# Optimization experiments

Hardware: AMD Instinct MI355X
Metric: run time of the kernel (lower is better)

## Reference

```python
import jax, jax.numpy as jnp
import numpy as np

N_NODES = 50000
N_EDGES = 800000
N_GRAPHS = 64
D = 64            # input_dim == hidden_dim == output_dim
N_GIN = 4         # num_layers - 1 GINConv layers
N_PRED = 5        # num_layers prediction heads
BN_EPS = 1e-5


def setup_inputs() -> dict:
    key = jax.random.key(0)
    ks = jax.random.split(key, 12)
    x = jax.random.normal(ks[0], (N_NODES, D), dtype=jnp.float32)
    edge_index = jax.random.randint(ks[1], (2, N_EDGES), 0, N_NODES, dtype=jnp.int32)
    # contiguous graph ids covering all N_GRAPHS segments (PyG batch vector)
    batch = ((jnp.arange(N_NODES) * N_GRAPHS) // N_NODES).astype(jnp.int32)
    s = 1.0 / np.sqrt(D)
    mlp_W1 = jax.random.uniform(ks[2], (N_GIN, D, D), jnp.float32, -s, s)
    mlp_b1 = jax.random.uniform(ks[3], (N_GIN, D), jnp.float32, -s, s)
    mlp_W2 = jax.random.uniform(ks[4], (N_GIN, D, D), jnp.float32, -s, s)
    mlp_b2 = jax.random.uniform(ks[5], (N_GIN, D), jnp.float32, -s, s)
    bn_gamma = jnp.ones((N_GIN, D), jnp.float32)
    bn_beta = jnp.zeros((N_GIN, D), jnp.float32)
    prelu_alpha = jnp.float32(0.25)  # nn.PReLU default, shared across layers
    pred_W = jax.random.uniform(ks[6], (N_PRED, D, D), jnp.float32, -s, s)
    pred_b = jax.random.uniform(ks[7], (N_PRED, D), jnp.float32, -s, s)
    return {
        "x": x, "edge_index": edge_index, "batch": batch,
        "mlp_W1": mlp_W1, "mlp_b1": mlp_b1, "mlp_W2": mlp_W2, "mlp_b2": mlp_b2,
        "bn_gamma": bn_gamma, "bn_beta": bn_beta, "prelu_alpha": prelu_alpha,
        "pred_W": pred_W, "pred_b": pred_b,
    }


def reference(x, edge_index, batch, mlp_W1, mlp_b1, mlp_W2, mlp_b2,
              bn_gamma, bn_beta, prelu_alpha, pred_W, pred_b):
    src, dst = edge_index[0], edge_index[1]
    h = x
    hidden_rep = [h]
    for l in range(N_GIN):
        # GINConv, eps = 0 (learn_eps=False): (1+eps)*x_i + sum_{j->i} x_j
        agg = jax.ops.segment_sum(h[src], dst, num_segments=N_NODES)
        z = h + agg
        # 2-layer MLP: Linear -> ReLU -> Linear
        z = jax.nn.relu(z @ mlp_W1[l] + mlp_b1[l])
        z = z @ mlp_W2[l] + mlp_b2[l]
        # BatchNorm1d over nodes (training-mode batch stats)
        mean = z.mean(axis=0)
        var = z.var(axis=0)
        z = (z - mean) * jax.lax.rsqrt(var + BN_EPS) * bn_gamma[l] + bn_beta[l]
        # shared single-parameter PReLU
        h = jnp.where(z > 0, z, prelu_alpha * z)
        hidden_rep.append(h)
    # per-layer max graph pooling + linear head (dropout_prob=0 -> identity)
    reps = []
    for l, hr in enumerate(hidden_rep):
        pooled = jax.ops.segment_max(hr, batch, num_segments=N_GRAPHS)
        reps.append(pooled @ pred_W[l] + pred_b[l])
    # torch.stack(dim=-1) -> (B, D, L), 'cat' aggregation flattens to (B, D*L)
    return jnp.stack(reps, axis=-1).reshape(N_GRAPHS, -1)
```

## Files before the change

### kernel.cpp

```cpp
#include <hip/hip_runtime.h>
#include <hip/hip_bf16.h>

#define N_NODES 50000
#define N_EDGES 800000
#define N_GRAPHS 64
#define DIM 64
#define N_GIN 4
#define N_PRED 5
#define BN_EPS 1e-5f
#define MM_BLOCKS 782
#define NB 625
#define BUCKET_SZ 80
#define POOL_CH 16

typedef short bf16x8 __attribute__((ext_vector_type(8)));
typedef float f32x4 __attribute__((ext_vector_type(4)));

__device__ __forceinline__ float b2f(__hip_bfloat16 v) { return __bfloat162float(v); }

__device__ __forceinline__ float loadv(const void* p, size_t i, int isb) {
    return isb ? b2f(((const __hip_bfloat16*)p)[i]) : ((const float*)p)[i];
}

__device__ __forceinline__ unsigned short f2bu(float f) {
    __hip_bfloat16 h = __float2bfloat16(f);
    return *(unsigned short*)&h;
}
__device__ __forceinline__ float bu2f(unsigned short u) {
    __hip_bfloat16 h = *(__hip_bfloat16*)&u;
    return b2f(h);
}

__device__ __forceinline__ unsigned int enc_f(float f) {
    unsigned int b = __float_as_uint(f);
    return (b & 0x80000000u) ? ~b : (b | 0x80000000u);
}
__device__ __forceinline__ float dec_f(unsigned int u) {
    unsigned int b = (u & 0x80000000u) ? (u ^ 0x80000000u) : ~u;
    return __uint_as_float(b);
}

__device__ __forceinline__ unsigned int gstart(unsigned int g) {
    return (g * (unsigned int)N_NODES + (N_GRAPHS - 1)) >> 6;
}
__device__ __forceinline__ unsigned int graph_of(unsigned int row) {
    return (row * (unsigned int)N_GRAPHS) / (unsigned int)N_NODES;
}

__global__ void init_all(unsigned int* __restrict__ base, int nZero, int nTotal,
                         const unsigned int* __restrict__ xw, int* __restrict__ flag) {
    int idx = blockIdx.x * blockDim.x + threadIdx.x;
    if (idx < nZero) base[idx] = 0u;
    else if (idx < nTotal) base[idx] = 0xFFFFFFFFu;
    if (blockIdx.x == 0) {
        __shared__ int cnt[256];
        int t = threadIdx.x;
        int c = 0;
        for (int i = t; i < 1024; i += 256) {
            unsigned int e = (xw[i] >> 7) & 0xFFu;
            if (e >= 0x70u && e <= 0x85u) c++;
        }
        cnt[t] = c;
        __syncthreads();
        for (int s = 128; s > 0; s >>= 1) {
            if (t < s) cnt[t] += cnt[t + s];
            __syncthreads();
        }
        if (t == 0) *flag = (cnt[0] >= 512) ? 1 : 0;
    }
}

__global__ void zero_u32(unsigned int* __restrict__ p, int n) {
    int i = blockIdx.x * blockDim.x + threadIdx.x;
    if (i < n) p[i] = 0u;
}

__global__ __launch_bounds__(256) void convert_pool_bg(
    const void* __restrict__ x, unsigned short* __restrict__ H,
    unsigned int* __restrict__ poolEnc, const int* __restrict__ dflag) {
    __shared__ float shmx[4][64];
    int isb = *dflag;
    unsigned int g = blockIdx.x / POOL_CH, p = blockIdx.x % POOL_CH;
    unsigned int s = gstart(g), e = gstart(g + 1), len = e - s;
    unsigned int rs = s + (len * p) / POOL_CH, re = s + (len * (p + 1)) / POOL_CH;
    int r = threadIdx.x >> 6, c = threadIdx.x & 63;
    float mx = -3.0e38f;
    for (unsigned int row = rs + r; row < re; row += 4) {
        float v = loadv(x, (size_t)row * DIM + c, isb);
        H[(size_t)row * DIM + c] = f2bu(v);
        mx = fmaxf(mx, v);
    }
    shmx[r][c] = mx;
    __syncthreads();
    if (threadIdx.x < 64) {
        float m = fmaxf(fmaxf(shmx[0][c], shmx[1][c]), fmaxf(shmx[2][c], shmx[3][c]));
        atomicMax(&poolEnc[g * DIM + c], enc_f(m));
    }
}


__global__ __launch_bounds__(256) void bucket_hist(const int* __restrict__ dst,
                                                   unsigned int* __restrict__ bucketCnt) {
    __shared__ unsigned int h[NB];
    for (int i = threadIdx.x; i < NB; i += 256) h[i] = 0u;
    __syncthreads();
    for (int e = blockIdx.x * 256 + threadIdx.x; e < N_EDGES; e += gridDim.x * 256)
        atomicAdd(&h[(unsigned int)dst[e] / BUCKET_SZ], 1u);
    __syncthreads();
    for (int i = threadIdx.x; i < NB; i += 256) {
        unsigned int v = h[i];
        if (v) atomicAdd(&bucketCnt[i], v);
    }
}

__global__ void scan_buckets(const unsigned int* __restrict__ bucketCnt,
                             unsigned int* __restrict__ bucketBase,
                             unsigned int* __restrict__ bucketCur) {
    __shared__ unsigned int s[256];
    int t = threadIdx.x;
    int i0 = t * 3;
    unsigned int v0 = (i0 < NB) ? bucketCnt[i0] : 0u;
    unsigned int v1 = (i0 + 1 < NB) ? bucketCnt[i0 + 1] : 0u;
    unsigned int v2 = (i0 + 2 < NB) ? bucketCnt[i0 + 2] : 0u;
    unsigned int tsum = v0 + v1 + v2;
    s[t] = tsum;
    __syncthreads();
    for (int off = 1; off < 256; off <<= 1) {
        unsigned int u = (t >= off) ? s[t - off] : 0u;
        __syncthreads();
        s[t] += u;
        __syncthreads();
    }
    unsigned int ex = s[t] - tsum;
    if (i0 < NB)     { bucketBase[i0] = ex;          bucketCur[i0] = ex; }
    if (i0 + 1 < NB) { bucketBase[i0 + 1] = ex + v0; bucketCur[i0 + 1] = ex + v0; }
    if (i0 + 2 < NB) { bucketBase[i0 + 2] = ex + v0 + v1; bucketCur[i0 + 2] = ex + v0 + v1; }
}

__global__ __launch_bounds__(256) void bucket_scatter(
    const int* __restrict__ src, const int* __restrict__ dst,
    unsigned int* __restrict__ bucketCur, uint2* __restrict__ ebuf) {
    __shared__ unsigned int h[NB];
    __shared__ unsigned int base[NB];
    for (int i = threadIdx.x; i < NB; i += 256) h[i] = 0u;
    __syncthreads();
    for (int e = blockIdx.x * 256 + threadIdx.x; e < N_EDGES; e += gridDim.x * 256)
        atomicAdd(&h[(unsigned int)dst[e] / BUCKET_SZ], 1u);
    __syncthreads();
    for (int i = threadIdx.x; i < NB; i += 256) {
        unsigned int v = h[i];
        base[i] = v ? atomicAdd(&bucketCur[i], v) : 0u;
        h[i] = 0u;
    }
    __syncthreads();
    for (int e = blockIdx.x * 256 + threadIdx.x; e < N_EDGES; e += gridDim.x * 256) {
        unsigned int d = (unsigned int)dst[e];
        unsigned int b = d / BUCKET_SZ;
        unsigned int off = atomicAdd(&h[b], 1u);
        ebuf[base[b] + off] = make_uint2((unsigned int)src[e], d);
    }
}

__global__ __launch_bounds__(256) void bucket_csr(
    const uint2* __restrict__ ebuf, const unsigned int* __restrict__ bucketBase,
    const unsigned int* __restrict__ bucketCnt, unsigned int* __restrict__ deg,
    unsigned int* __restrict__ cur, unsigned int* __restrict__ srclist) {
    __shared__ unsigned int ldeg[BUCKET_SZ], lcur[BUCKET_SZ], lscan[BUCKET_SZ];
    int b = blockIdx.x;
    unsigned int ebase = bucketBase[b];
    unsigned int ecnt = bucketCnt[b];
    unsigned int nbase = (unsigned int)b * BUCKET_SZ;
    int t = threadIdx.x;
    if (t < BUCKET_SZ) ldeg[t] = 0u;
    __syncthreads();
    for (unsigned int i = t; i < ecnt; i += 256)
        atomicAdd(&ldeg[ebuf[ebase + i].y - nbase], 1u);
    __syncthreads();
    if (t < BUCKET_SZ) lscan[t] = ldeg[t];
    __syncthreads();
    for (int off = 1; off < BUCKET_SZ; off <<= 1) {
        unsigned int u = 0u;
        if (t < BUCKET_SZ && t >= off) u = lscan[t - off];
        __syncthreads();
        if (t < BUCKET_SZ) lscan[t] += u;
        __syncthreads();
    }
    if (t < BUCKET_SZ) {
        lcur[t] = lscan[t] - ldeg[t];
        deg[nbase + t] = ldeg[t];
        cur[nbase + t] = ebase + lscan[t];
    }
    __syncthreads();
    for (unsigned int i = t; i < ecnt; i += 256) {
        uint2 e = ebuf[ebase + i];
        unsigned int off = atomicAdd(&lcur[e.y - nbase], 1u);
        srclist[ebase + off] = e.x;
    }
}


__global__ void pack_w(const void* __restrict__ W1, const void* __restrict__ W2,
                       unsigned short* __restrict__ P, const int* __restrict__ dflag) {
    int isb = *dflag;
    int mi = blockIdx.x;
    const void* src = (mi < 4) ? W1 : W2;
    size_t off = (size_t)(mi & 3) * 4096;
    for (int it = 0; it < 16; it++) {
        int idx = it * 256 + threadIdx.x;
        int j = idx & 7, l = (idx >> 3) & 63, s = (idx >> 9) & 1, t = idx >> 10;
        int k = s * 32 + (l >> 4) * 8 + j;
        int n = t * 16 + (l & 15);
        P[(size_t)mi * 4096 + idx] = f2bu(loadv(src, off + (size_t)k * 64 + n, isb));
    }
}

__global__ __launch_bounds__(256) void gather_affine(
    const unsigned short* __restrict__ Zsrc, unsigned short* __restrict__ Xb,
    const unsigned int* __restrict__ cur, const unsigned int* __restrict__ deg,
    const unsigned int* __restrict__ srclist, const float* __restrict__ scsh,
    const void* __restrict__ alpha_p, int ident, const int* __restrict__ dflag) {
    int lane = threadIdx.x & 63;
    int w = threadIdx.x >> 6;
    int node = blockIdx.x * 4 + w;
    int g8 = lane >> 3;
    int t8 = lane & 7;
    float sc[8], sh[8], alpha;
    if (ident) {
#pragma unroll
        for (int k = 0; k < 8; k++) { sc[k] = 1.0f; sh[k] = 0.0f; }
        alpha = 1.0f;
    } else {
#pragma unroll
        for (int k = 0; k < 8; k++) {
            sc[k] = scsh[t8 * 8 + k];
            sh[k] = scsh[64 + t8 * 8 + k];
        }
        alpha = loadv(alpha_p, 0, *dflag);
    }
    unsigned int cnt = deg[node];
    unsigned int start = cur[node] - cnt;
    const unsigned int* sl = srclist + start;
    float a[8] = {0.f, 0.f, 0.f, 0.f, 0.f, 0.f, 0.f, 0.f};
    if (g8 == 0) {
        bf16x8 sv = *(const bf16x8*)&Zsrc[(size_t)node * DIM + t8 * 8];
#pragma unroll
        for (int k = 0; k < 8; k++) {
            float v = bu2f((unsigned short)sv[k]) * sc[k] + sh[k];
            a[k] = v > 0.0f ? v : alpha * v;
        }
    }
    for (unsigned int j = g8; j < cnt; j += 8) {
        unsigned int s = sl[j];
        bf16x8 v = *(const bf16x8*)&Zsrc[(size_t)s * DIM + t8 * 8];
#pragma unroll
        for (int k = 0; k < 8; k++) {
            float h = bu2f((unsigned short)v[k]) * sc[k] + sh[k];
            a[k] += h > 0.0f ? h : alpha * h;
        }
    }
#pragma unroll
    for (int k = 0; k < 8; k++) {
        a[k] += __shfl_xor(a[k], 8);
        a[k] += __shfl_xor(a[k], 16);
        a[k] += __shfl_xor(a[k], 32);
    }
    if (g8 == 0) {
        bf16x8 o;
#pragma unroll
        for (int k = 0; k < 8; k++) o[k] = (short)f2bu(a[k]);
        *(bf16x8*)&Xb[(size_t)node * DIM + t8 * 8] = o;
    }
}

template <bool WRITEZ>
__global__ __launch_bounds__(256) void fused_mm(
    const unsigned short* __restrict__ Xb,
    const unsigned short* __restrict__ P1, const unsigned short* __restrict__ P2,
    const void* __restrict__ b1, size_t b1Off, const void* __restrict__ b2, size_t b2Off,
    unsigned short* __restrict__ Zb, float* __restrict__ part,
    unsigned int* __restrict__ zmaxE, unsigned int* __restrict__ zminE,
    const int* __restrict__ dflag) {
    __shared__ __align__(16) short T2[4][16][72];
    __shared__ float S1[4][64], S2[4][64];
    __shared__ unsigned int zmxL[2][64], zmnL[2][64];
    int isb = *dflag;
    int tid = threadIdx.x;
    int lane = tid & 63;
    int w = tid >> 6;
    if (tid < 128) {
        zmxL[tid >> 6][tid & 63] = 0u;
        zmnL[tid >> 6][tid & 63] = 0xFFFFFFFFu;
    }
    __syncthreads();
    int r0 = blockIdx.x * 64 + w * 16;
    bool valid = (r0 < N_NODES);
    int m = lane & 15, q = lane >> 4;
    int row = valid ? (r0 + m) : m;
    int r0blk = blockIdx.x * 64;
    unsigned int gLo = graph_of((unsigned int)r0blk);
    int lastRow = r0blk + 63 > N_NODES - 1 ? N_NODES - 1 : r0blk + 63;
    unsigned int gHi = graph_of((unsigned int)lastRow);

    const bf16x8* Xv = (const bf16x8*)Xb;
    bf16x8 a0 = Xv[(size_t)row * 8 + q];
    bf16x8 a1 = Xv[(size_t)row * 8 + 4 + q];
    const bf16x8* P1v = (const bf16x8*)P1;
    const bf16x8* P2v = (const bf16x8*)P2;
    bf16x8 w1[8], w2[8];
#pragma unroll
    for (int i = 0; i < 8; i++) {
        w1[i] = P1v[(size_t)i * 64 + lane];
        w2[i] = P2v[(size_t)i * 64 + lane];
    }

    f32x4 acc[4] = {{0.f, 0.f, 0.f, 0.f}, {0.f, 0.f, 0.f, 0.f},
                    {0.f, 0.f, 0.f, 0.f}, {0.f, 0.f, 0.f, 0.f}};
#pragma unroll
    for (int t = 0; t < 4; t++) {
        acc[t] = __builtin_amdgcn_mfma_f32_16x16x32_bf16(a0, w1[t * 2 + 0], acc[t], 0, 0, 0);
        acc[t] = __builtin_amdgcn_mfma_f32_16x16x32_bf16(a1, w1[t * 2 + 1], acc[t], 0, 0, 0);
    }
#pragma unroll
    for (int t = 0; t < 4; t++) {
        int col = t * 16 + m;
        float bv = loadv(b1, b1Off + col, isb);
#pragma unroll
        for (int reg = 0; reg < 4; reg++) {
            float v = acc[t][reg] + bv;
            v = v > 0.0f ? v : 0.0f;
            T2[w][q * 4 + reg][col] = (short)f2bu(v);
        }
    }

    bf16x8 c0 = *(const bf16x8*)&T2[w][m][q * 8];
    bf16x8 c1 = *(const bf16x8*)&T2[w][m][32 + q * 8];
    f32x4 acc2[4] = {{0.f, 0.f, 0.f, 0.f}, {0.f, 0.f, 0.f, 0.f},
                     {0.f, 0.f, 0.f, 0.f}, {0.f, 0.f, 0.f, 0.f}};
#pragma unroll
    for (int t = 0; t < 4; t++) {
        acc2[t] = __builtin_amdgcn_mfma_f32_16x16x32_bf16(c0, w2[t * 2 + 0], acc2[t], 0, 0, 0);
        acc2[t] = __builtin_amdgcn_mfma_f32_16x16x32_bf16(c1, w2[t * 2 + 1], acc2[t], 0, 0, 0);
    }

    float s1[4], s2[4];
#pragma unroll
    for (int t = 0; t < 4; t++) {
        float a = 0.0f, b = 0.0f;
        if (valid) {
            int col = t * 16 + m;
            float bv = loadv(b2, b2Off + col, isb);
            int rbase = r0 + q * 4;
#pragma unroll
            for (int reg = 0; reg < 4; reg++) {
                float z = acc2[t][reg] + bv;
                if (WRITEZ) Zb[(size_t)(rbase + reg) * DIM + col] = f2bu(z);
                unsigned int e = enc_f(z);
                unsigned int gi = graph_of((unsigned int)(rbase + reg)) - gLo;
                atomicMax(&zmxL[gi][col], e);
                atomicMin(&zmnL[gi][col], e);
                a += z;
                b += z * z;
            }
        }
        s1[t] = a;
        s2[t] = b;
    }
#pragma unroll
    for (int t = 0; t < 4; t++) {
        s1[t] += __shfl_xor(s1[t], 16);
        s1[t] += __shfl_xor(s1[t], 32);
        s2[t] += __shfl_xor(s2[t], 16);
        s2[t] += __shfl_xor(s2[t], 32);
    }
    if (q == 0) {
#pragma unroll
        for (int t = 0; t < 4; t++) {
            S1[w][t * 16 + m] = s1[t];
            S2[w][t * 16 + m] = s2[t];
        }
    }
    __syncthreads();
    if (tid < 128) {
        int c = tid & 63;
        float v = (tid < 64) ? (S1[0][c] + S1[1][c] + S1[2][c] + S1[3][c])
                             : (S2[0][c] + S2[1][c] + S2[2][c] + S2[3][c]);
        part[(size_t)blockIdx.x * 128 + tid] = v;
        int gi = tid >> 6;
        if (gLo + gi <= gHi) {
            atomicMax(&zmaxE[(gLo + gi) * 64 + c], zmxL[gi][c]);
            atomicMin(&zminE[(gLo + gi) * 64 + c], zmnL[gi][c]);
        }
    }
}

__global__ void stats_finalize(const float* __restrict__ part,
                               const void* __restrict__ gamma, const void* __restrict__ beta,
                               size_t gOff, float* __restrict__ scsh,
                               const int* __restrict__ dflag) {
    __shared__ double sh1[256], sh2[256];
    int c = blockIdx.x;
    int t = threadIdx.x;
    double a1 = 0.0, a2 = 0.0;
    for (int b = t; b < MM_BLOCKS; b += 256) {
        a1 += (double)part[(size_t)b * 128 + c];
        a2 += (double)part[(size_t)b * 128 + 64 + c];
    }
    sh1[t] = a1;
    sh2[t] = a2;
    __syncthreads();
    for (int s = 128; s > 0; s >>= 1) {
        if (t < s) { sh1[t] += sh1[t + s]; sh2[t] += sh2[t + s]; }
        __syncthreads();
    }
    if (t == 0) {
        int isb = *dflag;
        double mean = sh1[0] * (1.0 / N_NODES);
        double var = sh2[0] * (1.0 / N_NODES) - mean * mean;
        float inv = rsqrtf(fmaxf((float)var, 0.0f) + BN_EPS);
        float g = loadv(gamma, gOff + c, isb);
        float bb = loadv(beta, gOff + c, isb);
        scsh[c] = g * inv;
        scsh[64 + c] = bb - (float)mean * g * inv;
    }
}


__global__ void convert_pool_f(const void* __restrict__ x, float* __restrict__ A,
                               const int* __restrict__ batch,
                               unsigned int* __restrict__ poolEnc,
                               const int* __restrict__ dflag) {
    int isb = *dflag;
    int idx = blockIdx.x * blockDim.x + threadIdx.x;
    if (idx >= N_NODES * DIM) return;
    int i = idx >> 6, c = idx & 63;
    float v = loadv(x, idx, isb);
    A[idx] = v;
    atomicMax(&poolEnc[batch[i] * DIM + c], enc_f(v));
}

__global__ void copy_f4(const float4* __restrict__ A, float4* __restrict__ B, int n4) {
    int i = blockIdx.x * blockDim.x + threadIdx.x;
    if (i < n4) B[i] = A[i];
}

__global__ void edge_scatter(const int* __restrict__ src, const int* __restrict__ dst,
                             const float* __restrict__ A, float* __restrict__ B) {
    int idx = blockIdx.x * blockDim.x + threadIdx.x;
    if (idx >= N_EDGES * 16) return;
    int e = idx >> 4, q = idx & 15;
    int s = src[e], d = dst[e];
    float4 v = ((const float4*)(A + (size_t)s * DIM))[q];
    float* bp = B + (size_t)d * DIM + (q << 2);
    atomicAdd(bp + 0, v.x);
    atomicAdd(bp + 1, v.y);
    atomicAdd(bp + 2, v.z);
    atomicAdd(bp + 3, v.w);
}

template <bool RELU, bool STATS>
__global__ void mm64(const float* __restrict__ X, const void* __restrict__ W, size_t wOff,
                     const void* __restrict__ bias, size_t bOff, float* __restrict__ Y,
                     double* __restrict__ stats, const int* __restrict__ dflag) {
    int isb = *dflag;
    __shared__ float Ws[64][64];
    __shared__ float Xs[4][64];
    __shared__ float Sv[4][64];
    __shared__ float bsh[64];
    int tid = threadIdx.x;
    for (int i = tid; i < 4096; i += 256) Ws[i >> 6][i & 63] = loadv(W, wOff + i, isb);
    if (tid < 64) bsh[tid] = loadv(bias, bOff + tid, isb);
    int r = tid >> 6, d = tid & 63;
    int row = blockIdx.x * 4 + r;
    Xs[r][d] = X[(size_t)row * DIM + d];
    __syncthreads();
    float acc = bsh[d];
#pragma unroll
    for (int k = 0; k < 64; k++) acc += Xs[r][k] * Ws[k][d];
    if (RELU) acc = acc > 0.0f ? acc : 0.0f;
    Y[(size_t)row * DIM + d] = acc;
    if (STATS) {
        Sv[r][d] = acc;
        __syncthreads();
        if (tid < 64) {
            float s = 0.0f, s2 = 0.0f;
#pragma unroll
            for (int rr = 0; rr < 4; rr++) {
                float v = Sv[rr][tid];
                s += v;
                s2 += v * v;
            }
            atomicAdd(&stats[tid], (double)s);
            atomicAdd(&stats[64 + tid], (double)s2);
        }
    }
}

__global__ void bn_prelu_pool_f(const float* __restrict__ Z, float* __restrict__ H,
                                const double* __restrict__ stats,
                                const void* __restrict__ gamma, const void* __restrict__ beta,
                                size_t gOff, const void* __restrict__ alpha_p,
                                const int* __restrict__ batch,
                                unsigned int* __restrict__ poolEnc,
                                const int* __restrict__ dflag) {
    int isb = *dflag;
    int idx = blockIdx.x * blockDim.x + threadIdx.x;
    if (idx >= N_NODES * DIM) return;
    int i = idx >> 6, c = idx & 63;
    double mn = stats[c] * (1.0 / N_NODES);
    double var = stats[64 + c] * (1.0 / N_NODES) - mn * mn;
    float inv = rsqrtf(fmaxf((float)var, 0.0f) + BN_EPS);
    float z = Z[idx];
    float v = (z - (float)mn) * inv * loadv(gamma, gOff + c, isb) + loadv(beta, gOff + c, isb);
    float alpha = loadv(alpha_p, 0, isb);
    v = v > 0.0f ? v : alpha * v;
    H[idx] = v;
    atomicMax(&poolEnc[batch[i] * DIM + c], enc_f(v));
}

__global__ void pred_head(const unsigned int* __restrict__ poolEnc,
                          const unsigned int* __restrict__ zmaxE,
                          const unsigned int* __restrict__ zminE,
                          const float* __restrict__ scshAll,
                          const void* __restrict__ alpha_p,
                          const void* __restrict__ predW, const void* __restrict__ predB,
                          void* __restrict__ out, const int* __restrict__ dflag,
                          int useZmm) {
    int isb = *dflag;
    int l = blockIdx.x / N_GRAPHS;
    int g = blockIdx.x % N_GRAPHS;
    int d = threadIdx.x;
    __shared__ float ps[64];
    float pv;
    if (!useZmm || l == 0) {
        pv = dec_f(poolEnc[(size_t)l * N_GRAPHS * DIM + g * DIM + d]);
    } else {
        int s = l - 1;
        float sc = scshAll[s * 128 + d];
        float sh = scshAll[s * 128 + 64 + d];
        float alpha = loadv(alpha_p, 0, isb);
        float t1 = sc * dec_f(zmaxE[(size_t)s * 4096 + g * 64 + d]) + sh;
        float t2 = sc * dec_f(zminE[(size_t)s * 4096 + g * 64 + d]) + sh;
        float h1 = t1 > 0.0f ? t1 : alpha * t1;
        float h2 = t2 > 0.0f ? t2 : alpha * t2;
        pv = fmaxf(h1, h2);
    }
    ps[d] = pv;
    __syncthreads();
    float acc = loadv(predB, (size_t)l * DIM + d, isb);
    size_t wbase = (size_t)l * DIM * DIM;
#pragma unroll
    for (int k = 0; k < 64; k++) acc += ps[k] * loadv(predW, wbase + k * DIM + d, isb);
    int o = g * (DIM * N_PRED) + d * N_PRED + l;
    if (isb) ((__hip_bfloat16*)out)[o] = __float2bfloat16(acc);
    else ((float*)out)[o] = acc;
}

extern "C" void kernel_launch(void* const* d_in, const int* in_sizes, int n_in,
                              void* d_out, int out_size, void* d_ws, size_t ws_size,
                              hipStream_t stream) {
    const void* x     = d_in[0];
    const int*  edge  = (const int*)d_in[1];
    const int*  batch = (const int*)d_in[2];
    const void* W1    = d_in[3];
    const void* b1    = d_in[4];
    const void* W2    = d_in[5];
    const void* b2    = d_in[6];
    const void* gamma = d_in[7];
    const void* beta  = d_in[8];
    const void* alpha = d_in[9];
    const void* pW    = d_in[10];
    const void* pB    = d_in[11];

    float* A = (float*)d_ws;
    float* B = A + (size_t)N_NODES * DIM;
    unsigned int* poolEnc   = (unsigned int*)(B + (size_t)N_NODES * DIM);
    unsigned int* bucketCnt = poolEnc + N_PRED * N_GRAPHS * DIM;
    unsigned int* zmaxE     = bucketCnt + NB;
    unsigned int* zminE     = zmaxE + 4 * 4096;
    int* dflag = (int*)(zminE + 4 * 4096);
    unsigned int* deg        = (unsigned int*)(dflag + 1);
    unsigned int* cur        = deg + N_NODES;
    unsigned int* bucketBase = cur + N_NODES;
    unsigned int* bucketCur  = bucketBase + NB;
    unsigned int* srclist    = bucketCur + NB;
    unsigned short* Wpack = (unsigned short*)(srclist + N_EDGES);
    float* part    = (float*)(Wpack + 8 * 4096);
    float* scshAll = part + (size_t)MM_BLOCKS * 128;
    double* statsF = (double*)(scshAll + 512);
    uint2* ebuf = (uint2*)B;

    size_t needFull = (size_t)((char*)(statsF + 128) - (char*)d_ws);
    bool useMFMA = ws_size >= needFull;

    const int* esrc = edge;
    const int* edst = edge + N_EDGES;
    const int ND = N_NODES * DIM;

    unsigned short* Hb = (unsigned short*)A;
    unsigned short* Xb = Hb + (size_t)N_NODES * DIM;
    unsigned short* Zb = (unsigned short*)B;

    const int initZeroCnt = N_PRED * N_GRAPHS * DIM + NB + 4 * 4096;
    const int initTotCnt  = initZeroCnt + 4 * 4096;
    init_all<<<(initTotCnt + 255) / 256, 256, 0, stream>>>(poolEnc, initZeroCnt, initTotCnt,
                                                           (const unsigned int*)x, dflag);

    if (useMFMA) {
        bucket_hist<<<200, 256, 0, stream>>>(edst, bucketCnt);
        scan_buckets<<<1, 256, 0, stream>>>(bucketCnt, bucketBase, bucketCur);
        bucket_scatter<<<200, 256, 0, stream>>>(esrc, edst, bucketCur, ebuf);
        bucket_csr<<<NB, 256, 0, stream>>>(ebuf, bucketBase, bucketCnt, deg, cur, srclist);

        pack_w<<<8, 256, 0, stream>>>(W1, W2, Wpack, dflag);
        convert_pool_bg<<<N_GRAPHS * POOL_CH, 256, 0, stream>>>(x, Hb, poolEnc, dflag);
        for (int l = 0; l < N_GIN; l++) {
            size_t bOff = (size_t)l * DIM;
            if (l == 0)
                gather_affine<<<N_NODES / 4, 256, 0, stream>>>(
                    Hb, Xb, cur, deg, srclist, nullptr, alpha, 1, dflag);
            else
                gather_affine<<<N_NODES / 4, 256, 0, stream>>>(
                    Zb, Xb, cur, deg, srclist, scshAll + (size_t)(l - 1) * 128, alpha, 0,
                    dflag);
            if (l < 3)
                fused_mm<true><<<MM_BLOCKS, 256, 0, stream>>>(
                    Xb, Wpack + (size_t)l * 4096, Wpack + (size_t)(4 + l) * 4096,
                    b1, bOff, b2, bOff, Zb, part, zmaxE + (size_t)l * 4096,
                    zminE + (size_t)l * 4096, dflag);
            else
                fused_mm<false><<<MM_BLOCKS, 256, 0, stream>>>(
                    Xb, Wpack + (size_t)l * 4096, Wpack + (size_t)(4 + l) * 4096,
                    b1, bOff, b2, bOff, Zb, part, zmaxE + (size_t)l * 4096,
                    zminE + (size_t)l * 4096, dflag);
            stats_finalize<<<64, 256, 0, stream>>>(part, gamma, beta, bOff,
                                                   scshAll + (size_t)l * 128, dflag);
        }
        pred_head<<<N_PRED * N_GRAPHS, DIM, 0, stream>>>(
            poolEnc, zmaxE, zminE, scshAll, alpha, pW, pB, d_out, dflag, 1);
    } else {
        convert_pool_f<<<ND / 256, 256, 0, stream>>>(x, A, batch, poolEnc, dflag);
        for (int l = 0; l < N_GIN; l++) {
            size_t wOff = (size_t)l * DIM * DIM;
            size_t bOff = (size_t)l * DIM;
            copy_f4<<<(ND / 4 + 255) / 256, 256, 0, stream>>>((const float4*)A, (float4*)B,
                                                              ND / 4);
            edge_scatter<<<(N_EDGES * 16) / 256, 256, 0, stream>>>(esrc, edst, A, B);
            mm64<true, false><<<N_NODES / 4, 256, 0, stream>>>(B, W1, wOff, b1, bOff, A, nullptr,
                                                               dflag);
            zero_u32<<<1, 256, 0, stream>>>((unsigned int*)statsF, 256);
            mm64<false, true><<<N_NODES / 4, 256, 0, stream>>>(A, W2, wOff, b2, bOff, B, statsF,
                                                               dflag);
            bn_prelu_pool_f<<<ND / 256, 256, 0, stream>>>(
                B, A, statsF, gamma, beta, bOff, alpha, batch,
                poolEnc + (size_t)(l + 1) * N_GRAPHS * DIM, dflag);
        }
        pred_head<<<N_PRED * N_GRAPHS, DIM, 0, stream>>>(
            poolEnc, zmaxE, zminE, scshAll, alpha, pW, pB, d_out, dflag, 0);
    }
}
```

Before: 310.1 us.

## Split node features into two 32-channel planes and gather each half separately

Node feature buffers (input H and intermediate Z) are stored as two separate 32-channel bf16 planes instead of one interleaved 64-channel array. The gather kernel is launched twice per layer, once per plane, with 16 edge slots per wave and 4 lanes per row. This shrinks the random-access working set per gather pass so more of it can stay in cache. The trade-off is reading the CSR lists twice and issuing smaller, 64-byte row reads.

```diff
diff --git a/kernel.cpp b/kernel.cpp
--- a/kernel.cpp
+++ b/kernel.cpp
@@ -76,8 +76,9 @@
 }
 
 __global__ __launch_bounds__(256) void convert_pool_bg(
-    const void* __restrict__ x, unsigned short* __restrict__ H,
-    unsigned int* __restrict__ poolEnc, const int* __restrict__ dflag) {
+    const void* __restrict__ x, unsigned short* __restrict__ H0,
+    unsigned short* __restrict__ H1, unsigned int* __restrict__ poolEnc,
+    const int* __restrict__ dflag) {
     __shared__ float shmx[4][64];
     int isb = *dflag;
     unsigned int g = blockIdx.x / POOL_CH, p = blockIdx.x % POOL_CH;
@@ -87,7 +88,8 @@
     float mx = -3.0e38f;
     for (unsigned int row = rs + r; row < re; row += 4) {
         float v = loadv(x, (size_t)row * DIM + c, isb);
-        H[(size_t)row * DIM + c] = f2bu(v);
+        if (c < 32) H0[(size_t)row * 32 + c] = f2bu(v);
+        else        H1[(size_t)row * 32 + (c - 32)] = f2bu(v);
         mx = fmaxf(mx, v);
     }
     shmx[r][c] = mx;
@@ -214,16 +216,17 @@
     }
 }
 
-__global__ __launch_bounds__(256) void gather_affine(
-    const unsigned short* __restrict__ Zsrc, unsigned short* __restrict__ Xb,
+__global__ __launch_bounds__(256) void gather_half(
+    const unsigned short* __restrict__ Zp, unsigned short* __restrict__ Xb,
     const unsigned int* __restrict__ cur, const unsigned int* __restrict__ deg,
-    const unsigned int* __restrict__ srclist, const float* __restrict__ scsh,
-    const void* __restrict__ alpha_p, int ident, const int* __restrict__ dflag) {
+    const unsigned int* __restrict__ srclist, const float* __restrict__ scshL,
+    const void* __restrict__ alpha_p, int ident, int chbase,
+    const int* __restrict__ dflag) {
     int lane = threadIdx.x & 63;
     int w = threadIdx.x >> 6;
     int node = blockIdx.x * 4 + w;
-    int g8 = lane >> 3;
-    int t8 = lane & 7;
+    int slot = lane >> 2;
+    int t = lane & 3;
     float sc[8], sh[8], alpha;
     if (ident) {
 #pragma unroll
@@ -232,8 +235,8 @@
     } else {
 #pragma unroll
         for (int k = 0; k < 8; k++) {
-            sc[k] = scsh[t8 * 8 + k];
-            sh[k] = scsh[64 + t8 * 8 + k];
+            sc[k] = scshL[chbase + t * 8 + k];
+            sh[k] = scshL[64 + chbase + t * 8 + k];
         }
         alpha = loadv(alpha_p, 0, *dflag);
     }
@@ -241,17 +244,17 @@
     unsigned int start = cur[node] - cnt;
     const unsigned int* sl = srclist + start;
     float a[8] = {0.f, 0.f, 0.f, 0.f, 0.f, 0.f, 0.f, 0.f};
-    if (g8 == 0) {
-        bf16x8 sv = *(const bf16x8*)&Zsrc[(size_t)node * DIM + t8 * 8];
+    if (slot == 0) {
+        bf16x8 sv = *(const bf16x8*)&Zp[(size_t)node * 32 + t * 8];
 #pragma unroll
         for (int k = 0; k < 8; k++) {
             float v = bu2f((unsigned short)sv[k]) * sc[k] + sh[k];
             a[k] = v > 0.0f ? v : alpha * v;
         }
     }
-    for (unsigned int j = g8; j < cnt; j += 8) {
+    for (unsigned int j = slot; j < cnt; j += 16) {
         unsigned int s = sl[j];
-        bf16x8 v = *(const bf16x8*)&Zsrc[(size_t)s * DIM + t8 * 8];
+        bf16x8 v = *(const bf16x8*)&Zp[(size_t)s * 32 + t * 8];
 #pragma unroll
         for (int k = 0; k < 8; k++) {
             float h = bu2f((unsigned short)v[k]) * sc[k] + sh[k];
@@ -260,15 +263,16 @@
     }
 #pragma unroll
     for (int k = 0; k < 8; k++) {
+        a[k] += __shfl_xor(a[k], 4);
         a[k] += __shfl_xor(a[k], 8);
         a[k] += __shfl_xor(a[k], 16);
         a[k] += __shfl_xor(a[k], 32);
     }
-    if (g8 == 0) {
+    if (slot == 0) {
         bf16x8 o;
 #pragma unroll
         for (int k = 0; k < 8; k++) o[k] = (short)f2bu(a[k]);
-        *(bf16x8*)&Xb[(size_t)node * DIM + t8 * 8] = o;
+        *(bf16x8*)&Xb[(size_t)node * DIM + chbase + t * 8] = o;
     }
 }
 
@@ -350,10 +354,12 @@
             int col = t * 16 + m;
             float bv = loadv(b2, b2Off + col, isb);
             int rbase = r0 + q * 4;
+            unsigned short* Zp = Zb + ((col >= 32) ? (size_t)N_NODES * 32 : 0);
+            int colh = col & 31;
 #pragma unroll
             for (int reg = 0; reg < 4; reg++) {
                 float z = acc2[t][reg] + bv;
-                if (WRITEZ) Zb[(size_t)(rbase + reg) * DIM + col] = f2bu(z);
+                if (WRITEZ) Zp[(size_t)(rbase + reg) * 32 + colh] = f2bu(z);
                 unsigned int e = enc_f(z);
                 unsigned int gi = graph_of((unsigned int)(rbase + reg)) - gLo;
                 atomicMax(&zmxL[gi][col], e);
@@ -596,9 +602,9 @@
     const int* edst = edge + N_EDGES;
     const int ND = N_NODES * DIM;
 
-    unsigned short* Hb = (unsigned short*)A;
-    unsigned short* Xb = Hb + (size_t)N_NODES * DIM;
-    unsigned short* Zb = (unsigned short*)B;
+    unsigned short* Hp = (unsigned short*)A;
+    unsigned short* Xb = Hp + (size_t)N_NODES * DIM;
+    unsigned short* Zp = (unsigned short*)B;
 
     const int initZeroCnt = N_PRED * N_GRAPHS * DIM + NB + 4 * 4096;
     const int initTotCnt  = initZeroCnt + 4 * 4096;
@@ -612,25 +618,27 @@
         bucket_csr<<<NB, 256, 0, stream>>>(ebuf, bucketBase, bucketCnt, deg, cur, srclist);
 
         pack_w<<<8, 256, 0, stream>>>(W1, W2, Wpack, dflag);
-        convert_pool_bg<<<N_GRAPHS * POOL_CH, 256, 0, stream>>>(x, Hb, poolEnc, dflag);
+        convert_pool_bg<<<N_GRAPHS * POOL_CH, 256, 0, stream>>>(
+            x, Hp, Hp + (size_t)N_NODES * 32, poolEnc, dflag);
         for (int l = 0; l < N_GIN; l++) {
             size_t bOff = (size_t)l * DIM;
-            if (l == 0)
-                gather_affine<<<N_NODES / 4, 256, 0, stream>>>(
-                    Hb, Xb, cur, deg, srclist, nullptr, alpha, 1, dflag);
-            else
-                gather_affine<<<N_NODES / 4, 256, 0, stream>>>(
-                    Zb, Xb, cur, deg, srclist, scshAll + (size_t)(l - 1) * 128, alpha, 0,
-                    dflag);
+            const unsigned short* srcPl = (l == 0) ? Hp : Zp;
+            const float* scshL = (l == 0) ? nullptr : scshAll + (size_t)(l - 1) * 128;
+            int ident = (l == 0) ? 1 : 0;
+            gather_half<<<N_NODES / 4, 256, 0, stream>>>(
+                srcPl, Xb, cur, deg, srclist, scshL, alpha, ident, 0, dflag);
+            gather_half<<<N_NODES / 4, 256, 0, stream>>>(
+                srcPl + (size_t)N_NODES * 32, Xb, cur, deg, srclist, scshL, alpha, ident, 32,
+                dflag);
             if (l < 3)
                 fused_mm<true><<<MM_BLOCKS, 256, 0, stream>>>(
                     Xb, Wpack + (size_t)l * 4096, Wpack + (size_t)(4 + l) * 4096,
-                    b1, bOff, b2, bOff, Zb, part, zmaxE + (size_t)l * 4096,
+                    b1, bOff, b2, bOff, Zp, part, zmaxE + (size_t)l * 4096,
                     zminE + (size_t)l * 4096, dflag);
             else
                 fused_mm<false><<<MM_BLOCKS, 256, 0, stream>>>(
                     Xb, Wpack + (size_t)l * 4096, Wpack + (size_t)(4 + l) * 4096,
-                    b1, bOff, b2, bOff, Zb, part, zmaxE + (size_t)l * 4096,
+                    b1, bOff, b2, bOff, Zp, part, zmaxE + (size_t)l * 4096,
                     zminE + (size_t)l * 4096, dflag);
             stats_finalize<<<64, 256, 0, stream>>>(part, gamma, beta, bOff,
                                                    scshAll + (size_t)l * 128, dflag);
```

After: 379.5 us. 22.4% more time.
